# Optimization experiments

Measured on AMD Instinct MI355X. Metric: run time of the kernel, lower is better.

The kernel has to match this reference:

```python
import jax, jax.numpy as jnp
import numpy as np

N, E = 50000, 800000
IN_DIM, HIDDEN, LATENT = 128, 256, 64


def setup_inputs() -> dict:
    key = jax.random.key(0)
    ks = jax.random.split(key, 10)
    def lin(k, fan_in, fan_out):
        s = 1.0 / np.sqrt(fan_in)
        return jax.random.uniform(k, (fan_in, fan_out), jnp.float32, -s, s)
    x = jax.random.normal(ks[0], (N, IN_DIM), jnp.float32)
    edge_index = jax.random.randint(ks[1], (2, E), 0, N, jnp.int64)
    return {
        "x": x,
        "edge_index": edge_index,
        # enc1: SAGEConv(in_dim, hidden): lin_l (neighbors, with bias), lin_r (root, no bias)
        "W1l": lin(ks[2], IN_DIM, HIDDEN),
        "b1": jnp.zeros((HIDDEN,), jnp.float32),
        "W1r": lin(ks[3], IN_DIM, HIDDEN),
        # enc2: SAGEConv(hidden, latent)
        "W2l": lin(ks[4], HIDDEN, LATENT),
        "b2": jnp.zeros((LATENT,), jnp.float32),
        "W2r": lin(ks[5], HIDDEN, LATENT),
        # decoder Linear(latent, in_dim)
        "Wd": lin(ks[6], LATENT, IN_DIM),
        "bd": jax.random.uniform(ks[7], (IN_DIM,), jnp.float32, -1.0 / np.sqrt(LATENT), 1.0 / np.sqrt(LATENT)),
    }


def _sage_conv(x, src, dst, Wl, b, Wr, num_nodes):
    # PyG SAGEConv (aggr='mean'): out = lin_l(mean_{j in N(i)} x_j) + lin_r(x_i)
    summed = jax.ops.segment_sum(x[src], dst, num_segments=num_nodes)   # [N, d]
    cnt = jax.ops.segment_sum(jnp.ones((src.shape[0],), x.dtype), dst, num_segments=num_nodes)
    mean = summed / jnp.maximum(cnt, 1.0)[:, None]
    return mean @ Wl + b + x @ Wr


def reference(x, edge_index, W1l, b1, W1r, W2l, b2, W2r, Wd, bd):
    src, dst = edge_index[0], edge_index[1]
    n = x.shape[0]
    h = jax.nn.relu(_sage_conv(x, src, dst, W1l, b1, W1r, n))
    z = _sage_conv(h, src, dst, W2l, b2, W2r, n)
    x_hat = z @ Wd + bd
    return (z, x_hat)
```

## Files before the change

kernel.cpp:

```cpp
#include <hip/hip_runtime.h>
#include <stdint.h>

#define NN 50000
#define NE 800000
#define NB 196
#define NBK 196
#define NBUK 196
#define CHK 4096
#define MTOT (NBUK * NBK)
#define MSB 151
#define CVTB 6250
#define PREPB 418

typedef __bf16 bf16x8 __attribute__((ext_vector_type(8)));
typedef float f32x4 __attribute__((ext_vector_type(4)));
typedef unsigned short ushort_t;

__device__ inline float bf2f(uint16_t u) {
    union { uint32_t i; float f; } v; v.i = ((uint32_t)u) << 16; return v.f;
}
__device__ inline uint16_t f2bf(float f) {
    uint32_t u = __float_as_uint(f);
    u += 0x7fffu + ((u >> 16) & 1u);
    return (uint16_t)(u >> 16);
}
__device__ inline float rdf(const void* p, int i, int bf) {
    return bf ? bf2f(((const ushort_t*)p)[i]) : ((const float*)p)[i];
}

__device__ inline int blk_or(int v, int* flag) {
    if (threadIdx.x == 0) *flag = 0;
    __syncthreads();
    if (v) atomicOr(flag, 1);
    __syncthreads();
    return *flag;
}
__device__ inline int detect_sh(const int* __restrict__ ei, int* flag) {
    int t = threadIdx.x;
    int v = ei[2 * t + 1] | ei[2 * (t + 256) + 1] | ei[2 * (t + 512) + 1] | ei[2 * (t + 768) + 1];
    return blk_or(v, flag) ? 0 : 1;
}
__device__ inline int detect_bf(const ushort_t* __restrict__ xw, int* flag) {
    int t = threadIdx.x;
    int bad = 0;
#pragma unroll
    for (int r = 0; r < 2; ++r) {
        uint16_t w = xw[t + 256 * r];
        int e = (w >> 7) & 0xFF;
        if (!(w == 0 || (e >= 96 && e <= 144))) bad = 1;
    }
    return blk_or(bad, flag) ? 0 : 1;
}

__global__ __launch_bounds__(256) void k_stage1(const int* __restrict__ ei, const void* __restrict__ x,
                                                const void* __restrict__ W1l, const void* __restrict__ W1r,
                                                const void* __restrict__ W2l, const void* __restrict__ W2r,
                                                const void* __restrict__ Wd,
                                                const void* __restrict__ b1, const void* __restrict__ b2,
                                                const void* __restrict__ bd,
                                                int* __restrict__ cntm, ushort_t* __restrict__ xb,
                                                ushort_t* __restrict__ wt, ushort_t* __restrict__ w2lt,
                                                ushort_t* __restrict__ w2rt, ushort_t* __restrict__ wdt,
                                                float* __restrict__ b1f, float* __restrict__ b2f,
                                                float* __restrict__ bdf) {
    __shared__ int flag;
    int b = blockIdx.x, t = threadIdx.x;
    if (b < NBK) {
        int sh = detect_sh(ei, &flag);
        __shared__ int hist[NBUK];
        if (t < NBUK) hist[t] = 0;
        __syncthreads();
        for (int i = t; i < CHK; i += 256) {
            int e = b * CHK + i;
            if (e < NE) {
                int d = ei[(size_t)(NE + e) << sh];
                atomicAdd(&hist[d >> 8], 1);
            }
        }
        __syncthreads();
        if (t < NBUK) cntm[t * NBK + b] = hist[t];
    } else if (b < NBK + CVTB) {
        int bf = detect_bf((const ushort_t*)x, &flag);
        int i = (b - NBK) * 256 + t;
        if (bf) {
            reinterpret_cast<ushort4*>(xb)[i] = reinterpret_cast<const ushort4*>(x)[i];
        } else {
            float4 v = reinterpret_cast<const float4*>(x)[i];
            ushort4 o;
            o.x = f2bf(v.x); o.y = f2bf(v.y); o.z = f2bf(v.z); o.w = f2bf(v.w);
            reinterpret_cast<ushort4*>(xb)[i] = o;
        }
    } else {
        int bf = detect_bf((const ushort_t*)x, &flag);
        int idx = (b - NBK - CVTB) * 256 + t;
        if (idx < 65536) {
            int c = idx >> 8, k = idx & 255;
            float v = (k < 128) ? rdf(W1l, k * 256 + c, bf) : rdf(W1r, (k - 128) * 256 + c, bf);
            wt[c * 256 + k] = f2bf(v);
        } else if (idx < 81920) {
            int t2 = idx - 65536;
            int c = t2 >> 8, k = t2 & 255;
            w2lt[c * 256 + k] = f2bf(rdf(W2l, k * 64 + c, bf));
        } else if (idx < 98304) {
            int t2 = idx - 81920;
            int c = t2 >> 8, k = t2 & 255;
            w2rt[c * 256 + k] = f2bf(rdf(W2r, k * 64 + c, bf));
        } else if (idx < 106496) {
            int t2 = idx - 98304;
            int c = t2 >> 6, k = t2 & 63;
            wdt[c * 64 + k] = f2bf(rdf(Wd, k * 128 + c, bf));
        } else if (idx < 106752) {
            b1f[idx - 106496] = rdf(b1, idx - 106496, bf);
        } else if (idx < 106816) {
            b2f[idx - 106752] = rdf(b2, idx - 106752, bf);
        } else if (idx < 106944) {
            bdf[idx - 106816] = rdf(bd, idx - 106816, bf);
        }
    }
}

__device__ inline int block_scan256(int v, int* ws, int* btot) {
    int lane = threadIdx.x & 63, wv = threadIdx.x >> 6;
    int incl = v;
#pragma unroll
    for (int d = 1; d < 64; d <<= 1) {
        int n = __shfl_up(incl, d);
        if (lane >= d) incl += n;
    }
    if (lane == 63) ws[wv] = incl;
    __syncthreads();
    if (threadIdx.x == 0) {
        int r = 0;
#pragma unroll
        for (int k = 0; k < 4; ++k) { int t = ws[k]; ws[k] = r; r += t; }
        *btot = r;
    }
    __syncthreads();
    return ws[wv] + incl - v;
}

__global__ __launch_bounds__(256) void k_scanMA(const int* __restrict__ cntm, int* __restrict__ offm,
                                                int* __restrict__ bsM) {
    __shared__ int ws[4]; __shared__ int btot;
    int i = blockIdx.x * 256 + threadIdx.x;
    int v = (i < MTOT) ? cntm[i] : 0;
    int excl = block_scan256(v, ws, &btot);
    if (i < MTOT) offm[i] = excl;
    if (threadIdx.x == 0) bsM[blockIdx.x] = btot;
}

__global__ __launch_bounds__(256) void k_scanMC2(int* __restrict__ offm, const int* __restrict__ bsM) {
    __shared__ int red[256];
    int t = threadIdx.x, b = blockIdx.x;
    red[t] = (t < b) ? bsM[t] : 0;
    __syncthreads();
#pragma unroll
    for (int s = 128; s > 0; s >>= 1) {
        if (t < s) red[t] += red[t + s];
        __syncthreads();
    }
    int boff = red[0];
    int i = b * 256 + t;
    if (i < MTOT) offm[i] += boff;
}

__global__ __launch_bounds__(256) void k_scatterC(const int* __restrict__ ei,
                                                  const int* __restrict__ offm, uint32_t* __restrict__ pairs) {
    __shared__ int cur[NBUK];
    __shared__ int flag;
    int t = threadIdx.x, blk = blockIdx.x;
    int sh = detect_sh(ei, &flag);
    if (t < NBUK) cur[t] = offm[t * NBK + blk];
    __syncthreads();
    for (int i = t; i < CHK; i += 256) {
        int e = blk * CHK + i;
        if (e < NE) {
            int s = ei[(size_t)e << sh];
            int d = ei[(size_t)(NE + e) << sh];
            int pos = atomicAdd(&cur[d >> 8], 1);
            pairs[pos] = (uint32_t)s | ((uint32_t)(d & 255) << 16);
        }
    }
}

__global__ __launch_bounds__(256) void k_d1s(const uint32_t* __restrict__ pairs, const int* __restrict__ offm,
                                             int* __restrict__ rowptr, int* __restrict__ blocksum) {
    __shared__ int hist[256];
    __shared__ int ws[4]; __shared__ int btot;
    int t = threadIdx.x, b = blockIdx.x;
    hist[t] = 0;
    __syncthreads();
    int beg = offm[b * NBK];
    int end = (b + 1 < NBUK) ? offm[(b + 1) * NBK] : NE;
    for (int i = beg + t; i < end; i += 256) {
        uint32_t p = pairs[i];
        atomicAdd(&hist[p >> 16], 1);
    }
    __syncthreads();
    int v = hist[t];
    int excl = block_scan256(v, ws, &btot);
    int node = b * 256 + t;
    if (node < NN) rowptr[node] = excl;
    if (t == 0) blocksum[b] = btot;
}

__global__ __launch_bounds__(256) void k_scanC2(int* __restrict__ rowptr, const int* __restrict__ blocksum) {
    __shared__ int red[256];
    int t = threadIdx.x, b = blockIdx.x;
    red[t] = (t < b && t < NB) ? blocksum[t] : 0;
    __syncthreads();
#pragma unroll
    for (int s = 128; s > 0; s >>= 1) {
        if (t < s) red[t] += red[t + s];
        __syncthreads();
    }
    int boff = red[0];
    int i = b * 256 + t;
    if (i < NN) rowptr[i] += boff;
    if (b == 0 && t == 0) rowptr[NN] = NE;
}

__global__ __launch_bounds__(256) void k_d2(const uint32_t* __restrict__ pairs, const int* __restrict__ offm,
                                            const int* __restrict__ rowptr, ushort_t* __restrict__ srclist) {
    __shared__ int cur[256];
    int t = threadIdx.x, b = blockIdx.x;
    int node = b * 256 + t;
    cur[t] = (node < NN) ? rowptr[node] : 0;
    __syncthreads();
    int beg = offm[b * NBK];
    int end = (b + 1 < NBUK) ? offm[(b + 1) * NBK] : NE;
    for (int i = beg + t; i < end; i += 256) {
        uint32_t p = pairs[i];
        int pos = atomicAdd(&cur[p >> 16], 1);
        srclist[pos] = (ushort_t)(p & 0xffff);
    }
}

__global__ __launch_bounds__(256) void k_agg128(const ushort_t* __restrict__ xb, const int* __restrict__ rowptr,
                                                const ushort_t* __restrict__ srclist, ushort_t* __restrict__ out) {
    int node = (blockIdx.x * 256 + threadIdx.x) >> 6;
    int lane = threadIdx.x & 63;
    if (node >= NN) return;
    int beg = rowptr[node], end = rowptr[node + 1];
    float a0 = 0.f, a1 = 0.f;
    int j = beg;
    for (; j + 7 < end; j += 8) {
        uint32_t p[8];
#pragma unroll
        for (int u = 0; u < 8; ++u) {
            int s = srclist[j + u];
            p[u] = *reinterpret_cast<const uint32_t*>(xb + (size_t)s * 128 + lane * 2);
        }
#pragma unroll
        for (int u = 0; u < 8; ++u) {
            a0 += bf2f((uint16_t)(p[u] & 0xffff));
            a1 += bf2f((uint16_t)(p[u] >> 16));
        }
    }
    for (; j + 3 < end; j += 4) {
        uint32_t p[4];
#pragma unroll
        for (int u = 0; u < 4; ++u) {
            int s = srclist[j + u];
            p[u] = *reinterpret_cast<const uint32_t*>(xb + (size_t)s * 128 + lane * 2);
        }
#pragma unroll
        for (int u = 0; u < 4; ++u) {
            a0 += bf2f((uint16_t)(p[u] & 0xffff));
            a1 += bf2f((uint16_t)(p[u] >> 16));
        }
    }
    for (; j < end; ++j) {
        int s = srclist[j];
        uint32_t p = *reinterpret_cast<const uint32_t*>(xb + (size_t)s * 128 + lane * 2);
        a0 += bf2f((uint16_t)(p & 0xffff));
        a1 += bf2f((uint16_t)(p >> 16));
    }
    float inv = 1.0f / (float)max(end - beg, 1);
    uint32_t o = (uint32_t)f2bf(a0 * inv) | ((uint32_t)f2bf(a1 * inv) << 16);
    *reinterpret_cast<uint32_t*>(out + (size_t)node * 128 + lane * 2) = o;
}

__global__ __launch_bounds__(256, 2) void k_gemm12(const ushort_t* __restrict__ meanx, const ushort_t* __restrict__ xb,
                                                   const ushort_t* __restrict__ wt, const float* __restrict__ b1f,
                                                   const ushort_t* __restrict__ w2lt, const ushort_t* __restrict__ w2rt,
                                                   const float* __restrict__ b2f,
                                                   ushort_t* __restrict__ y, float* __restrict__ r) {
    __shared__ alignas(16) ushort_t ht[16 * 256];
    int wv = threadIdx.x >> 6, lane = threadIdx.x & 63;
    int m = lane & 15, q = lane >> 4;
    bf16x8 B1[8][4];
#pragma unroll
    for (int ks = 0; ks < 8; ++ks) {
        int kb = ks * 32 + q * 8;
#pragma unroll
        for (int ct = 0; ct < 4; ++ct)
            B1[ks][ct] = *reinterpret_cast<const bf16x8*>(wt + (size_t)(wv * 64 + ct * 16 + m) * 256 + kb);
    }
    int op = wv >> 1;
    int cb = (wv & 1) * 32;
    const ushort_t* wtx = op ? w2rt : w2lt;
    bf16x8 B2[8][2];
#pragma unroll
    for (int ks = 0; ks < 8; ++ks) {
        int kb = ks * 32 + q * 8;
#pragma unroll
        for (int ct = 0; ct < 2; ++ct)
            B2[ks][ct] = *reinterpret_cast<const bf16x8*>(wtx + (size_t)(cb + ct * 16 + m) * 256 + kb);
    }
    float bias2[2];
#pragma unroll
    for (int ct = 0; ct < 2; ++ct) bias2[ct] = b2f[cb + ct * 16 + m];

    const int ntiles = NN / 16;
    for (int t = blockIdx.x; t < ntiles; t += gridDim.x) {
        int r0 = t * 16;
        int row = r0 + m;
        f32x4 acc[4];
#pragma unroll
        for (int ct = 0; ct < 4; ++ct) acc[ct] = (f32x4){0.f, 0.f, 0.f, 0.f};
#pragma unroll
        for (int ks = 0; ks < 8; ++ks) {
            int kb = ks * 32 + q * 8;
            const ushort_t* ap = (ks < 4) ? (meanx + (size_t)row * 128 + kb)
                                          : (xb + (size_t)row * 128 + (kb - 128));
            bf16x8 a = *reinterpret_cast<const bf16x8*>(ap);
#pragma unroll
            for (int ct = 0; ct < 4; ++ct)
                acc[ct] = __builtin_amdgcn_mfma_f32_16x16x32_bf16(a, B1[ks][ct], acc[ct], 0, 0, 0);
        }
#pragma unroll
        for (int ct = 0; ct < 4; ++ct) {
            int c = wv * 64 + ct * 16 + m;
            float bias = b1f[c];
#pragma unroll
            for (int i = 0; i < 4; ++i) {
                int lr = q * 4 + i;
                int off = (lr * 512 + c * 2) ^ ((lr & 7) << 4);
                *reinterpret_cast<ushort_t*>(reinterpret_cast<char*>(ht) + off) =
                    f2bf(fmaxf(acc[ct][i] + bias, 0.f));
            }
        }
        __syncthreads();
        f32x4 acc2[2];
        acc2[0] = (f32x4){0.f, 0.f, 0.f, 0.f}; acc2[1] = acc2[0];
#pragma unroll
        for (int ks = 0; ks < 8; ++ks) {
            int boff = (m * 512 + ks * 64 + q * 16) ^ ((m & 7) << 4);
            bf16x8 a = *reinterpret_cast<const bf16x8*>(reinterpret_cast<const char*>(ht) + boff);
#pragma unroll
            for (int ct = 0; ct < 2; ++ct)
                acc2[ct] = __builtin_amdgcn_mfma_f32_16x16x32_bf16(a, B2[ks][ct], acc2[ct], 0, 0, 0);
        }
#pragma unroll
        for (int ct = 0; ct < 2; ++ct) {
            int c = cb + ct * 16 + m;
#pragma unroll
            for (int i = 0; i < 4; ++i) {
                int rr = r0 + q * 4 + i;
                if (op == 0) y[(size_t)rr * 64 + c] = f2bf(acc2[ct][i]);
                else         r[(size_t)rr * 64 + c] = acc2[ct][i] + bias2[ct];
            }
        }
        __syncthreads();
    }
}

__global__ __launch_bounds__(256) void k_agg2g3(const ushort_t* __restrict__ y, const int* __restrict__ rowptr,
                                                const ushort_t* __restrict__ srclist,
                                                float* zr,
                                                const ushort_t* __restrict__ wdt, const float* __restrict__ bdf,
                                                float* __restrict__ xhat) {
    __shared__ alignas(16) ushort_t zt[16][72];
    int b = blockIdx.x;
    int wv = threadIdx.x >> 6, lane = threadIdx.x & 63;
    int m = lane & 15, q = lane >> 4;
    bf16x8 B[2][2];
#pragma unroll
    for (int ks = 0; ks < 2; ++ks) {
        int kb = ks * 32 + q * 8;
#pragma unroll
        for (int ct = 0; ct < 2; ++ct)
            B[ks][ct] = *reinterpret_cast<const bf16x8*>(wdt + (size_t)(wv * 32 + ct * 16 + m) * 64 + kb);
    }
    float bias0 = bdf[wv * 32 + m], bias1 = bdf[wv * 32 + 16 + m];

    int half = lane >> 5, l32 = lane & 31;
#pragma unroll
    for (int s = 0; s < 4; ++s) {
        int node = b * 16 + wv * 4 + s;
        int beg = rowptr[node], end = rowptr[node + 1];
        float a0 = 0.f, a1 = 0.f;
        int j = beg + half;
        for (; j + 6 < end; j += 8) {
            uint32_t p[4];
#pragma unroll
            for (int u = 0; u < 4; ++u) {
                int sx = srclist[j + 2 * u];
                p[u] = *reinterpret_cast<const uint32_t*>(y + (size_t)sx * 64 + l32 * 2);
            }
#pragma unroll
            for (int u = 0; u < 4; ++u) {
                a0 += bf2f((uint16_t)(p[u] & 0xffff));
                a1 += bf2f((uint16_t)(p[u] >> 16));
            }
        }
        for (; j < end; j += 2) {
            int sx = srclist[j];
            uint32_t p = *reinterpret_cast<const uint32_t*>(y + (size_t)sx * 64 + l32 * 2);
            a0 += bf2f((uint16_t)(p & 0xffff));
            a1 += bf2f((uint16_t)(p >> 16));
        }
        a0 += __shfl_xor(a0, 32);
        a1 += __shfl_xor(a1, 32);
        if (half == 0) {
            float inv = 1.0f / (float)max(end - beg, 1);
            float2 rv = *reinterpret_cast<const float2*>(zr + (size_t)node * 64 + l32 * 2);
            float z0 = a0 * inv + rv.x;
            float z1 = a1 * inv + rv.y;
            float2 zo; zo.x = z0; zo.y = z1;
            *reinterpret_cast<float2*>(zr + (size_t)node * 64 + l32 * 2) = zo;
            uint32_t o = (uint32_t)f2bf(z0) | ((uint32_t)f2bf(z1) << 16);
            *reinterpret_cast<uint32_t*>(&zt[wv * 4 + s][l32 * 2]) = o;
        }
    }
    __syncthreads();
    f32x4 acc[2];
    acc[0] = (f32x4){0.f, 0.f, 0.f, 0.f}; acc[1] = acc[0];
#pragma unroll
    for (int ks = 0; ks < 2; ++ks) {
        bf16x8 a = *reinterpret_cast<const bf16x8*>(&zt[m][ks * 32 + q * 8]);
#pragma unroll
        for (int ct = 0; ct < 2; ++ct)
            acc[ct] = __builtin_amdgcn_mfma_f32_16x16x32_bf16(a, B[ks][ct], acc[ct], 0, 0, 0);
    }
#pragma unroll
    for (int ct = 0; ct < 2; ++ct) {
        int c = wv * 32 + ct * 16 + m;
        float bb = ct ? bias1 : bias0;
#pragma unroll
        for (int i = 0; i < 4; ++i) {
            int rr = b * 16 + q * 4 + i;
            xhat[(size_t)rr * 128 + c] = acc[ct][i] + bb;
        }
    }
}

extern "C" void kernel_launch(void* const* d_in, const int* in_sizes, int n_in,
                              void* d_out, int out_size, void* d_ws, size_t ws_size,
                              hipStream_t stream) {
    const void *px = nullptr, *pei = nullptr, *pW1l = nullptr, *pW1r = nullptr,
               *pW2l = nullptr, *pW2r = nullptr, *pWd = nullptr,
               *pb1 = nullptr, *pb2 = nullptr, *pbd = nullptr;
    for (int i = 0; i < n_in; ++i) {
        const void* p = d_in[i];
        switch (in_sizes[i]) {
            case 6400000: px  = p; break;
            case 1600000: pei = p; break;
            case 32768:   if (!pW1l) pW1l = p; else pW1r = p; break;
            case 16384:   if (!pW2l) pW2l = p; else pW2r = p; break;
            case 8192:    pWd = p; break;
            case 256:     pb1 = p; break;
            case 128:     pbd = p; break;
            case 64:      pb2 = p; break;
            default: break;
        }
    }
    if (!px || !pei || !pW1l || !pW1r || !pW2l || !pW2r || !pWd || !pb1 || !pb2 || !pbd) {
        px = d_in[0]; pei = d_in[1]; pW1l = d_in[2]; pb1 = d_in[3]; pW1r = d_in[4];
        pW2l = d_in[5]; pb2 = d_in[6]; pW2r = d_in[7]; pWd = d_in[8]; pbd = d_in[9];
    }
    const int* ei = (const int*)pei;

    char* base = (char*)d_ws;
    size_t off = 0;
    auto alloc = [&](size_t bytes) -> void* {
        void* r = base + off;
        off = (off + bytes + 255) & ~(size_t)255;
        return r;
    };
    int* rowptr   = (int*)alloc((size_t)(NN + 1) * 4);
    int* blocksum = (int*)alloc((size_t)NB * 4);
    int* cntm     = (int*)alloc((size_t)MTOT * 4);
    int* offm     = (int*)alloc((size_t)MTOT * 4);
    int* bsM      = (int*)alloc(256 * 4);
    uint32_t* pairs = (uint32_t*)alloc((size_t)NE * 4);
    ushort_t* srclist = (ushort_t*)alloc((size_t)NE * 2);
    ushort_t* wt   = (ushort_t*)alloc((size_t)65536 * 2);
    ushort_t* w2lt = (ushort_t*)alloc((size_t)16384 * 2);
    ushort_t* w2rt = (ushort_t*)alloc((size_t)16384 * 2);
    ushort_t* wdt  = (ushort_t*)alloc((size_t)8192 * 2);
    float* b1f    = (float*)alloc(256 * 4);
    float* b2f    = (float*)alloc(64 * 4);
    float* bdf    = (float*)alloc(128 * 4);
    ushort_t* xb  = (ushort_t*)alloc((size_t)NN * 128 * 2);
    ushort_t* y   = (ushort_t*)alloc((size_t)NN * 64 * 2);

    float* out_z    = (float*)d_out;
    float* out_xhat = out_z + (size_t)NN * 64;

    ushort_t* meanx = (ushort_t*)out_xhat;
    float*    rbuf  = out_z;

    k_stage1<<<NBK + CVTB + PREPB, 256, 0, stream>>>(ei, px, pW1l, pW1r, pW2l, pW2r, pWd, pb1, pb2, pbd,
                                                     cntm, xb, wt, w2lt, w2rt, wdt, b1f, b2f, bdf);

    k_scanMA<<<MSB, 256, 0, stream>>>(cntm, offm, bsM);
    k_scanMC2<<<MSB, 256, 0, stream>>>(offm, bsM);
    k_scatterC<<<NBK, 256, 0, stream>>>(ei, offm, pairs);
    k_d1s<<<NBUK, 256, 0, stream>>>(pairs, offm, rowptr, blocksum);
    k_scanC2<<<NB, 256, 0, stream>>>(rowptr, blocksum);
    k_d2<<<NBUK, 256, 0, stream>>>(pairs, offm, rowptr, srclist);

    int ab = (NN + 3) / 4;
    k_agg128<<<ab, 256, 0, stream>>>(xb, rowptr, srclist, meanx);

    k_gemm12<<<512, 256, 0, stream>>>(meanx, xb, wt, b1f, w2lt, w2rt, b2f, y, rbuf);
    k_agg2g3<<<NN / 16, 256, 0, stream>>>(y, rowptr, srclist, rbuf, wdt, bdf, out_xhat);
}
```

Measured before the change: 230.6 us.

## Fold block-offset scans into consumers and merge CSR histogram with fill

Drops the separate second-pass scan kernels by having each consumer block recompute the 151-entry block-sum prefix in shared memory and add it on the fly. The per-bucket histogram, row-pointer computation and srclist fill are merged into one kernel, since each bucket's global start is already known from the bucket offsets. Three launches and two global read-modify-write passes go away, at the cost of a small redundant scan per block and the pairs range being read twice inside one kernel.

```diff
diff --git a/kernel.cpp b/kernel.cpp
--- a/kernel.cpp
+++ b/kernel.cpp
@@ -149,28 +149,28 @@
     if (threadIdx.x == 0) bsM[blockIdx.x] = btot;
 }
 
-__global__ __launch_bounds__(256) void k_scanMC2(int* __restrict__ offm, const int* __restrict__ bsM) {
-    __shared__ int red[256];
-    int t = threadIdx.x, b = blockIdx.x;
-    red[t] = (t < b) ? bsM[t] : 0;
-    __syncthreads();
-#pragma unroll
-    for (int s = 128; s > 0; s >>= 1) {
-        if (t < s) red[t] += red[t + s];
-        __syncthreads();
-    }
-    int boff = red[0];
-    int i = b * 256 + t;
-    if (i < MTOT) offm[i] += boff;
+__device__ inline void bsm_prefix(const int* __restrict__ bsM, int* bsPre, int* ws, int* btot) {
+    int t = threadIdx.x;
+    int v = (t < MSB) ? bsM[t] : 0;
+    int excl = block_scan256(v, ws, &btot[0]);
+    bsPre[t] = excl;
+    __syncthreads();
 }
 
 __global__ __launch_bounds__(256) void k_scatterC(const int* __restrict__ ei,
-                                                  const int* __restrict__ offm, uint32_t* __restrict__ pairs) {
+                                                  const int* __restrict__ offm, const int* __restrict__ bsM,
+                                                  uint32_t* __restrict__ pairs) {
     __shared__ int cur[NBUK];
+    __shared__ int bsPre[256];
+    __shared__ int ws[4]; __shared__ int btot;
     __shared__ int flag;
     int t = threadIdx.x, blk = blockIdx.x;
     int sh = detect_sh(ei, &flag);
-    if (t < NBUK) cur[t] = offm[t * NBK + blk];
+    bsm_prefix(bsM, bsPre, ws, &btot);
+    if (t < NBUK) {
+        int g = t * NBK + blk;
+        cur[t] = offm[g] + bsPre[g >> 8];
+    }
     __syncthreads();
     for (int i = t; i < CHK; i += 256) {
         int e = blk * CHK + i;
@@ -183,15 +183,29 @@
     }
 }
 
-__global__ __launch_bounds__(256) void k_d1s(const uint32_t* __restrict__ pairs, const int* __restrict__ offm,
-                                             int* __restrict__ rowptr, int* __restrict__ blocksum) {
+__global__ __launch_bounds__(256) void k_d12(const uint32_t* __restrict__ pairs, const int* __restrict__ offm,
+                                             const int* __restrict__ bsM,
+                                             int* __restrict__ rowptr, ushort_t* __restrict__ srclist) {
     __shared__ int hist[256];
+    __shared__ int cur[256];
+    __shared__ int bsPre[256];
     __shared__ int ws[4]; __shared__ int btot;
     int t = threadIdx.x, b = blockIdx.x;
+    bsm_prefix(bsM, bsPre, ws, &btot);
+    __shared__ int sbeg, send;
+    if (t == 0) {
+        int g0 = b * NBK;
+        sbeg = offm[g0] + bsPre[g0 >> 8];
+        if (b + 1 < NBUK) {
+            int g1 = (b + 1) * NBK;
+            send = offm[g1] + bsPre[g1 >> 8];
+        } else {
+            send = NE;
+        }
+    }
     hist[t] = 0;
     __syncthreads();
-    int beg = offm[b * NBK];
-    int end = (b + 1 < NBUK) ? offm[(b + 1) * NBK] : NE;
+    int beg = sbeg, end = send;
     for (int i = beg + t; i < end; i += 256) {
         uint32_t p = pairs[i];
         atomicAdd(&hist[p >> 16], 1);
@@ -200,35 +214,11 @@
     int v = hist[t];
     int excl = block_scan256(v, ws, &btot);
     int node = b * 256 + t;
-    if (node < NN) rowptr[node] = excl;
-    if (t == 0) blocksum[b] = btot;
-}
-
-__global__ __launch_bounds__(256) void k_scanC2(int* __restrict__ rowptr, const int* __restrict__ blocksum) {
-    __shared__ int red[256];
-    int t = threadIdx.x, b = blockIdx.x;
-    red[t] = (t < b && t < NB) ? blocksum[t] : 0;
-    __syncthreads();
-#pragma unroll
-    for (int s = 128; s > 0; s >>= 1) {
-        if (t < s) red[t] += red[t + s];
-        __syncthreads();
-    }
-    int boff = red[0];
-    int i = b * 256 + t;
-    if (i < NN) rowptr[i] += boff;
+    int rp = beg + excl;
+    if (node < NN) rowptr[node] = rp;
+    cur[t] = rp;
     if (b == 0 && t == 0) rowptr[NN] = NE;
-}
-
-__global__ __launch_bounds__(256) void k_d2(const uint32_t* __restrict__ pairs, const int* __restrict__ offm,
-                                            const int* __restrict__ rowptr, ushort_t* __restrict__ srclist) {
-    __shared__ int cur[256];
-    int t = threadIdx.x, b = blockIdx.x;
-    int node = b * 256 + t;
-    cur[t] = (node < NN) ? rowptr[node] : 0;
-    __syncthreads();
-    int beg = offm[b * NBK];
-    int end = (b + 1 < NBUK) ? offm[(b + 1) * NBK] : NE;
+    __syncthreads();
     for (int i = beg + t; i < end; i += 256) {
         uint32_t p = pairs[i];
         int pos = atomicAdd(&cur[p >> 16], 1);
@@ -480,7 +470,6 @@
         return r;
     };
     int* rowptr   = (int*)alloc((size_t)(NN + 1) * 4);
-    int* blocksum = (int*)alloc((size_t)NB * 4);
     int* cntm     = (int*)alloc((size_t)MTOT * 4);
     int* offm     = (int*)alloc((size_t)MTOT * 4);
     int* bsM      = (int*)alloc(256 * 4);
@@ -506,11 +495,8 @@
                                                      cntm, xb, wt, w2lt, w2rt, wdt, b1f, b2f, bdf);
 
     k_scanMA<<<MSB, 256, 0, stream>>>(cntm, offm, bsM);
-    k_scanMC2<<<MSB, 256, 0, stream>>>(offm, bsM);
-    k_scatterC<<<NBK, 256, 0, stream>>>(ei, offm, pairs);
-    k_d1s<<<NBUK, 256, 0, stream>>>(pairs, offm, rowptr, blocksum);
-    k_scanC2<<<NB, 256, 0, stream>>>(rowptr, blocksum);
-    k_d2<<<NBUK, 256, 0, stream>>>(pairs, offm, rowptr, srclist);
+    k_scatterC<<<NBK, 256, 0, stream>>>(ei, offm, bsM, pairs);
+    k_d12<<<NBUK, 256, 0, stream>>>(pairs, offm, bsM, rowptr, srclist);
 
     int ab = (NN + 3) / 4;
     k_agg128<<<ab, 256, 0, stream>>>(xb, rowptr, srclist, meanx);
```

After: 223.8 us. -3.0%, faster.
